# Optimization experiments

Hardware: AMD Instinct MI355X
Metric: run time of the kernel (lower is better)

The kernel has to match this reference:

```python
import jax, jax.numpy as jnp
import numpy as np

N_NODES = 50000
N_EDGES = 800000
N_ATOMS = 100
HID = 128
N_LAYERS = 3
OUT_LAYERS = 2
OUT_DIM = 1
N_GRAPHS = 1024
EPS = 1e-12  # F.normalize eps


def setup_inputs() -> dict:
    key = jax.random.key(0)
    ks = jax.random.split(key, 12)
    s = 0.05
    x_ori = jax.random.randint(ks[0], (N_NODES,), 0, N_ATOMS)
    edge_index = jax.random.randint(ks[1], (2, N_EDGES), 0, N_NODES)
    edge_attr = jax.random.normal(ks[2], (N_EDGES, 1), jnp.float32)
    batch_ids = jnp.sort(jax.random.randint(ks[3], (N_NODES,), 0, N_GRAPHS))
    embd_w = jax.random.normal(ks[4], (N_ATOMS, HID), jnp.float32) * s
    gamma_w = jnp.ones((N_LAYERS, N_ATOMS, 1), jnp.float32)  # reset_parameters sets ones
    w_atom_W = jax.random.normal(ks[5], (N_LAYERS, HID, HID), jnp.float32) * s
    w_atom_b = jax.random.normal(ks[6], (N_LAYERS, HID), jnp.float32) * s
    lin_W = jax.random.normal(ks[7], (OUT_LAYERS, HID, HID), jnp.float32) * s
    lin_b = jax.random.normal(ks[8], (OUT_LAYERS, HID), jnp.float32) * s
    wp_W = jax.random.normal(ks[9], (HID, OUT_DIM), jnp.float32) * s
    wp_b = jax.random.normal(ks[10], (OUT_DIM,), jnp.float32) * s
    return dict(x_ori=x_ori, edge_index=edge_index, edge_attr=edge_attr,
                batch_ids=batch_ids, embd_w=embd_w, gamma_w=gamma_w,
                w_atom_W=w_atom_W, w_atom_b=w_atom_b, lin_W=lin_W, lin_b=lin_b,
                wp_W=wp_W, wp_b=wp_b)


def reference(x_ori, edge_index, edge_attr, batch_ids, embd_w, gamma_w,
              w_atom_W, w_atom_b, lin_W, lin_b, wp_W, wp_b):
    src, dst = edge_index[0], edge_index[1]
    x = embd_w[x_ori]  # [N, H]
    for l in range(N_LAYERS):
        h = jax.nn.relu(x @ w_atom_W[l] + w_atom_b[l])            # [N, H]
        gam = jax.nn.sigmoid(gamma_w[l])[x_ori][dst]              # [E, 1]
        ew = jnp.exp(-gam * edge_attr ** 2)                       # [E, 1]
        msg = ew * h[src]                                         # [E, H] gather+weight
        agg = jax.ops.segment_sum(msg, dst, num_segments=N_NODES) # scatter-add
        y = agg + x
        nrm = jnp.maximum(jnp.linalg.norm(y, axis=1, keepdims=True), EPS)
        x = y / nrm                                               # F.normalize(., 2, 1)
    for i in range(OUT_LAYERS):
        x = jax.nn.relu(x @ lin_W[i] + lin_b[i])
    m_x = jax.ops.segment_sum(x, batch_ids, num_segments=N_GRAPHS)  # [G, H]
    props = m_x @ wp_W + wp_b                                      # [G, 1]
    return jnp.squeeze(props, axis=1)                              # [G]
```

## Files before the change

### kernel.cpp

```cpp
#include <hip/hip_runtime.h>
#include <hip/hip_bf16.h>
#include <math.h>

typedef __hip_bfloat16 bf16;
typedef unsigned int uint;
typedef unsigned short ushort;
typedef __attribute__((ext_vector_type(8))) short short8;
typedef __attribute__((ext_vector_type(4))) float f32x4;

#define HID 128
#define NN 50000
#define NE 800000
#define NG 1024
#define NA 100
#define CAP 64

__device__ __forceinline__ uint bf16_rne_hi(float f) {
    uint u = __float_as_uint(f);
    return (u + 0x7fffu + ((u >> 16) & 1u)) & 0xffff0000u;
}
__device__ __forceinline__ uint pack_bf16x2(float lo, float hi) {
    return (bf16_rne_hi(lo) >> 16) | bf16_rne_hi(hi);
}
__device__ __forceinline__ ushort bf16_rne(float f) {
    uint u = __float_as_uint(f);
    return (ushort)((u + 0x7fffu + ((u >> 16) & 1u)) >> 16);
}
__device__ __forceinline__ float load_f(const void* p, int i, int f32) {
    return f32 ? ((const float*)p)[i]
               : __uint_as_float((uint)((const ushort*)p)[i] << 16);
}
__device__ __forceinline__ int detect_f32(const void* emb) {
    const ushort* p = (const ushort*)emb;
    int lane = threadIdx.x & 63;
    int bad0, bad1;
    {
        float v = __uint_as_float((uint)p[lane * 4] << 16);
        bad0 = (!(v == v) || fabsf(v) > 1e4f || (v != 0.0f && fabsf(v) < 1e-10f));
        float w = __uint_as_float((uint)p[lane * 4 + 2] << 16);
        bad1 = (!(w == w) || fabsf(w) > 1e4f || (w != 0.0f && fabsf(w) < 1e-10f));
    }
    int cnt = __popcll(__ballot(bad0)) + __popcll(__ballot(bad1));
    return cnt > 16;
}

#define EMB_BLKS   ((NN * 64) / 256)
#define PACKW_BLKS (5 * 16384 / 256)
#define CVT_CNT    (300 + 384 + 256 + 128 + 1)
#define CVT_BLKS   5
#define INITC_BLKS ((NN + 255) / 256)
#define PREP_B1    EMB_BLKS
#define PREP_B2    (PREP_B1 + PACKW_BLKS)
#define PREP_B3    (PREP_B2 + CVT_BLKS)
#define PREP_B4    (PREP_B3 + INITC_BLKS)
#define PREP_GRID  (PREP_B4 + 1)

__global__ void prep_k(const int* __restrict__ xo, const void* __restrict__ emb,
                       const void* __restrict__ gamw, const void* __restrict__ wAW,
                       const void* __restrict__ wAb, const void* __restrict__ linW,
                       const void* __restrict__ linb, const void* __restrict__ wpW,
                       const void* __restrict__ wpb,
                       uint* __restrict__ xb, ushort* __restrict__ Wp,
                       float* __restrict__ f_sgam, float* __restrict__ f_wAb,
                       float* __restrict__ f_linb, float* __restrict__ f_wp,
                       float* __restrict__ f_wpb, int* __restrict__ cursor,
                       int* __restrict__ flag) {
    int f32 = detect_f32(emb);
    int b = blockIdx.x, t = threadIdx.x;
    if (b < PREP_B1) {
        int g = b * 256 + t;
        int node = g >> 6, c2 = g & 63;
        int base = xo[node] * HID + c2 * 2;
        xb[g] = pack_bf16x2(load_f(emb, base, f32), load_f(emb, base + 1, f32));
    } else if (b < PREP_B2) {
        int t2 = (b - PREP_B1) * 256 + t;
        int i   = t2 & 7;
        int n   = (t2 >> 3) & 15;
        int q   = (t2 >> 7) & 3;
        int j16 = (t2 >> 9) & 7;
        int ks  = (t2 >> 12) & 3;
        int mat = t2 >> 14;
        int k = ks * 32 + q * 8 + i;
        int j = j16 * 16 + n;
        const void* W = (mat < 3) ? wAW : linW;
        int off = ((mat < 3) ? mat : (mat - 3)) * 16384 + k * HID + j;
        Wp[t2] = bf16_rne(load_f(W, off, f32));
    } else if (b < PREP_B3) {
        int idx = (b - PREP_B2) * 256 + t;
        if (idx < 300) {
            float v = load_f(gamw, idx, f32);
            f_sgam[idx] = 1.0f / (1.0f + __expf(-v));
        } else if (idx < 684) {
            f_wAb[idx - 300] = load_f(wAb, idx - 300, f32);
        } else if (idx < 940) {
            f_linb[idx - 684] = load_f(linb, idx - 684, f32);
        } else if (idx < 1068) {
            f_wp[idx - 940] = load_f(wpW, idx - 940, f32);
        } else if (idx < CVT_CNT) {
            f_wpb[0] = load_f(wpb, 0, f32);
        }
    } else if (b < PREP_B4) {
        int n = (b - PREP_B3) * 256 + t;
        if (n < NN) cursor[n] = n * CAP;
    } else {
        if (t == 0) *flag = f32;
    }
}

__global__ void scatter_k(const int* __restrict__ src, const int* __restrict__ dst,
                          const void* __restrict__ ea, int* __restrict__ cursor,
                          uint* __restrict__ csr, const int* __restrict__ flag) {
    int e0 = (blockIdx.x * blockDim.x + threadIdx.x) * 4;
    if (e0 >= NE) return;
    int4 s4 = *(const int4*)(src + e0);
    int4 d4 = *(const int4*)(dst + e0);
    float a0, a1, a2, a3;
    if (*flag) {
        float4 f = *(const float4*)((const float*)ea + e0);
        a0 = f.x; a1 = f.y; a2 = f.z; a3 = f.w;
    } else {
        ushort4 u = *(const ushort4*)((const ushort*)ea + e0);
        a0 = __uint_as_float((uint)u.x << 16);
        a1 = __uint_as_float((uint)u.y << 16);
        a2 = __uint_as_float((uint)u.z << 16);
        a3 = __uint_as_float((uint)u.w << 16);
    }
    int p0 = atomicAdd(&cursor[d4.x], 1);
    int p1 = atomicAdd(&cursor[d4.y], 1);
    int p2 = atomicAdd(&cursor[d4.z], 1);
    int p3 = atomicAdd(&cursor[d4.w], 1);
    if (p0 < d4.x * CAP + CAP) csr[p0] = (uint)(s4.x & 0xffff) | bf16_rne_hi(a0 * a0);
    if (p1 < d4.y * CAP + CAP) csr[p1] = (uint)(s4.y & 0xffff) | bf16_rne_hi(a1 * a1);
    if (p2 < d4.z * CAP + CAP) csr[p2] = (uint)(s4.z & 0xffff) | bf16_rne_hi(a2 * a2);
    if (p3 < d4.w * CAP + CAP) csr[p3] = (uint)(s4.w & 0xffff) | bf16_rne_hi(a3 * a3);
}

__global__ __launch_bounds__(256) void gemm_mfma_k(const uint* __restrict__ xb,
                                                   const ushort* __restrict__ Wp,
                                                   const float* __restrict__ bias,
                                                   uint* __restrict__ outb) {
    int wave = threadIdx.x >> 6;
    int lane = threadIdx.x & 63;
    int ln15 = lane & 15;
    int q    = lane >> 4;
    int m0   = blockIdx.x * 128 + wave * 32;
    int mA = min(m0 + ln15, NN - 1);
    int mB = min(m0 + 16 + ln15, NN - 1);

    const short8* A8 = (const short8*)xb;
    const short8* B8 = (const short8*)Wp;

    f32x4 acc0[8], acc1[8];
#pragma unroll
    for (int j16 = 0; j16 < 8; ++j16) {
        float bv = bias[j16 * 16 + ln15];
        acc0[j16] = (f32x4){bv, bv, bv, bv};
        acc1[j16] = acc0[j16];
    }
#pragma unroll
    for (int ks = 0; ks < 4; ++ks) {
        short8 a0 = A8[mA * 16 + ks * 4 + q];
        short8 a1 = A8[mB * 16 + ks * 4 + q];
#pragma unroll
        for (int j16 = 0; j16 < 8; ++j16) {
            short8 b = B8[(ks * 8 + j16) * 64 + q * 16 + ln15];
            acc0[j16] = __builtin_amdgcn_mfma_f32_16x16x32_bf16(a0, b, acc0[j16], 0, 0, 0);
            acc1[j16] = __builtin_amdgcn_mfma_f32_16x16x32_bf16(a1, b, acc1[j16], 0, 0, 0);
        }
    }
    ushort* ob = (ushort*)outb;
#pragma unroll
    for (int reg = 0; reg < 4; ++reg) {
        int n0 = m0 + q * 4 + reg;
        int n1 = n0 + 16;
#pragma unroll
        for (int j16 = 0; j16 < 8; ++j16) {
            if (n0 < NN)
                ob[(size_t)n0 * HID + j16 * 16 + ln15] = bf16_rne(fmaxf(acc0[j16][reg], 0.0f));
            if (n1 < NN)
                ob[(size_t)n1 * HID + j16 * 16 + ln15] = bf16_rne(fmaxf(acc1[j16][reg], 0.0f));
        }
    }
}

__global__ void gather_norm_k(const int* __restrict__ cursor, const uint* __restrict__ csr,
                              const int* __restrict__ xo, const float* __restrict__ sgam,
                              const uint* __restrict__ hb, uint* __restrict__ xb) {
    int n = blockIdx.x * 4 + (threadIdx.x >> 6);
    int lane = threadIdx.x & 63;
    int base = n * CAP;
    int deg = min(cursor[n] - base, CAP);
    const uint* cp = csr + base;
    float g = sgam[xo[n]];
    float ax = 0.0f, ay = 0.0f;
    for (int e = 0; e < deg; e += 8) {
        uint4 c0 = *(const uint4*)(cp + e);
        uint4 c1 = *(const uint4*)(cp + e + 4);
        uint cc[8];
        cc[0] = c0.x; cc[1] = c0.y; cc[2] = c0.z; cc[3] = c0.w;
        cc[4] = c1.x; cc[5] = c1.y; cc[6] = c1.z; cc[7] = c1.w;
#pragma unroll
        for (int i = 1; i < 8; ++i) cc[i] = (e + i < deg) ? cc[i] : cc[0];
        uint v[8];
#pragma unroll
        for (int i = 0; i < 8; ++i) v[i] = hb[(cc[i] & 0xffffu) * 64 + lane];
        float w[8];
#pragma unroll
        for (int i = 0; i < 8; ++i) {
            float we = __expf(-g * __uint_as_float(cc[i] & 0xffff0000u));
            w[i] = (e + i < deg) ? we : 0.0f;
        }
#pragma unroll
        for (int i = 0; i < 8; ++i) {
            ax = fmaf(w[i], __uint_as_float(v[i] << 16), ax);
            ay = fmaf(w[i], __uint_as_float(v[i] & 0xffff0000u), ay);
        }
    }
    uint xv = xb[n * 64 + lane];
    float yx = ax + __uint_as_float(xv << 16);
    float yy = ay + __uint_as_float(xv & 0xffff0000u);
    float ss = yx * yx + yy * yy;
#pragma unroll
    for (int m = 32; m; m >>= 1) ss += __shfl_xor(ss, m);
    float inv = 1.0f / fmaxf(sqrtf(ss), 1e-12f);
    xb[n * 64 + lane] = pack_bf16x2(yx * inv, yy * inv);
}

__global__ void graph_k(const uint* __restrict__ xb, const int* __restrict__ batch,
                        const float* __restrict__ wp, const float* __restrict__ wpb,
                        void* __restrict__ out, const int* __restrict__ flag) {
    int g = blockIdx.x, tid = threadIdx.x;
    int lo = 0, hi = NN;
    while (lo < hi) { int mid = (lo + hi) >> 1; if (batch[mid] < g) lo = mid + 1; else hi = mid; }
    int start = lo;
    hi = NN;
    while (lo < hi) { int mid = (lo + hi) >> 1; if (batch[mid] < g + 1) lo = mid + 1; else hi = mid; }
    int end = lo;
    int c2 = tid & 63, half = tid >> 6;
    float wp0 = wp[c2 * 2], wp1 = wp[c2 * 2 + 1];
    float acc = 0.0f;
    for (int n = start + half; n < end; n += 2) {
        uint v = xb[(size_t)n * 64 + c2];
        acc = fmaf(__uint_as_float(v << 16), wp0, acc);
        acc = fmaf(__uint_as_float(v & 0xffff0000u), wp1, acc);
    }
    __shared__ float red[128];
    red[tid] = acc;
    __syncthreads();
#pragma unroll
    for (int s = 64; s; s >>= 1) {
        if (tid < s) red[tid] += red[tid + s];
        __syncthreads();
    }
    if (tid == 0) {
        float r = red[0] + wpb[0];
        if (*flag) ((float*)out)[g] = r;
        else       ((bf16*)out)[g] = __float2bfloat16(r);
    }
}

extern "C" void kernel_launch(void* const* d_in, const int* in_sizes, int n_in,
                              void* d_out, int out_size, void* d_ws, size_t ws_size,
                              hipStream_t stream) {
    const int*  xo    = (const int*)d_in[0];
    const int*  ei    = (const int*)d_in[1];
    const int*  src   = ei;
    const int*  dst   = ei + NE;
    const void* ea    = d_in[2];
    const int*  batch = (const int*)d_in[3];
    const void* emb   = d_in[4];
    const void* gamw  = d_in[5];
    const void* wAW   = d_in[6];
    const void* wAb   = d_in[7];
    const void* linW  = d_in[8];
    const void* linb  = d_in[9];
    const void* wpW   = d_in[10];
    const void* wpb   = d_in[11];

    float* F = (float*)d_ws;
    uint*  xb     = (uint*)F;
    uint*  hb     = xb + (size_t)NN * 64;
    uint*  csr    = hb + (size_t)NN * 64;
    int*   cursor = (int*)(csr + (size_t)NN * CAP);
    float* P      = (float*)(cursor + NN + 7);
    float* f_sgam = P;
    float* f_wAb  = f_sgam + 304;
    float* f_linb = f_wAb + 384;
    float* f_wp   = f_linb + 256;
    float* f_wpb  = f_wp + 128;
    int*   flag   = (int*)(f_wpb + 8);
    ushort* Wp    = (ushort*)(flag + 8);

    prep_k<<<PREP_GRID, 256, 0, stream>>>(xo, emb, gamw, wAW, wAb, linW, linb, wpW, wpb,
                                          xb, Wp, f_sgam, f_wAb, f_linb, f_wp, f_wpb,
                                          cursor, flag);

    scatter_k<<<(NE / 4 + 255) / 256, 256, 0, stream>>>(src, dst, ea, cursor, csr, flag);

    const int gemm_grid = (NN + 127) / 128;
    for (int l = 0; l < 3; ++l) {
        gemm_mfma_k<<<gemm_grid, 256, 0, stream>>>(xb, Wp + l * 16384, f_wAb + l * HID, hb);
        gather_norm_k<<<NN / 4, 256, 0, stream>>>(cursor, csr, xo, f_sgam + l * NA,
                                                  hb, xb);
    }

    gemm_mfma_k<<<gemm_grid, 256, 0, stream>>>(xb, Wp + 3 * 16384, f_linb,       hb);
    gemm_mfma_k<<<gemm_grid, 256, 0, stream>>>(hb, Wp + 4 * 16384, f_linb + HID, xb);

    graph_k<<<NG, 128, 0, stream>>>(xb, batch, f_wp, f_wpb, d_out, flag);
}
```

Measured before the change: 324.0 us.

## Build CSR via two-pass shared-memory binning instead of global atomics

Replaces the per-edge global atomic scatter into the fixed-capacity CSR with two passes. The first pass stages edges in shared memory, grouped into 98 coarse destination buckets, and flushes each bucket to global memory with one atomic per bucket. The second pass has each block own a 128-node quarter of a bucket, builds its CSR slice with shared-memory atomics, and writes it out with coalesced stores. This is meant to cut the contention and scattered writes of global atomics. In exchange it adds an intermediate bin buffer, an extra kernel launch, and a redundant scan in which each of four blocks reads the whole bucket.

```diff
diff --git a/kernel.cpp b/kernel.cpp
--- a/kernel.cpp
+++ b/kernel.cpp
@@ -14,6 +14,11 @@
 #define NG 1024
 #define NA 100
 #define CAP 64
+
+#define NB   98
+#define BCAP 16384
+#define SCAP 32
+#define NN_PAD (NB * 512)
 
 __device__ __forceinline__ uint bf16_rne_hi(float f) {
     uint u = __float_as_uint(f);
@@ -46,14 +51,12 @@
 
 #define EMB_BLKS   ((NN * 64) / 256)
 #define PACKW_BLKS (5 * 16384 / 256)
-#define CVT_CNT    (300 + 384 + 256 + 128 + 1)
+#define CVT_CNT    (300 + 384 + 256 + 128 + 1 + NB)
 #define CVT_BLKS   5
-#define INITC_BLKS ((NN + 255) / 256)
 #define PREP_B1    EMB_BLKS
 #define PREP_B2    (PREP_B1 + PACKW_BLKS)
 #define PREP_B3    (PREP_B2 + CVT_BLKS)
-#define PREP_B4    (PREP_B3 + INITC_BLKS)
-#define PREP_GRID  (PREP_B4 + 1)
+#define PREP_GRID  (PREP_B3 + 1)
 
 __global__ void prep_k(const int* __restrict__ xo, const void* __restrict__ emb,
                        const void* __restrict__ gamw, const void* __restrict__ wAW,
@@ -63,7 +66,7 @@
                        uint* __restrict__ xb, ushort* __restrict__ Wp,
                        float* __restrict__ f_sgam, float* __restrict__ f_wAb,
                        float* __restrict__ f_linb, float* __restrict__ f_wp,
-                       float* __restrict__ f_wpb, int* __restrict__ cursor,
+                       float* __restrict__ f_wpb, int* __restrict__ gcur,
                        int* __restrict__ flag) {
     int f32 = detect_f32(emb);
     int b = blockIdx.x, t = threadIdx.x;
@@ -96,43 +99,94 @@
             f_linb[idx - 684] = load_f(linb, idx - 684, f32);
         } else if (idx < 1068) {
             f_wp[idx - 940] = load_f(wpW, idx - 940, f32);
+        } else if (idx < 1069) {
+            f_wpb[0] = load_f(wpb, 0, f32);
         } else if (idx < CVT_CNT) {
-            f_wpb[0] = load_f(wpb, 0, f32);
-        }
-    } else if (b < PREP_B4) {
-        int n = (b - PREP_B3) * 256 + t;
-        if (n < NN) cursor[n] = n * CAP;
+            gcur[idx - 1069] = (idx - 1069) * BCAP;
+        }
     } else {
         if (t == 0) *flag = f32;
     }
 }
 
-__global__ void scatter_k(const int* __restrict__ src, const int* __restrict__ dst,
-                          const void* __restrict__ ea, int* __restrict__ cursor,
-                          uint* __restrict__ csr, const int* __restrict__ flag) {
-    int e0 = (blockIdx.x * blockDim.x + threadIdx.x) * 4;
-    if (e0 >= NE) return;
-    int4 s4 = *(const int4*)(src + e0);
-    int4 d4 = *(const int4*)(dst + e0);
-    float a0, a1, a2, a3;
-    if (*flag) {
-        float4 f = *(const float4*)((const float*)ea + e0);
-        a0 = f.x; a1 = f.y; a2 = f.z; a3 = f.w;
-    } else {
-        ushort4 u = *(const ushort4*)((const ushort*)ea + e0);
-        a0 = __uint_as_float((uint)u.x << 16);
-        a1 = __uint_as_float((uint)u.y << 16);
-        a2 = __uint_as_float((uint)u.z << 16);
-        a3 = __uint_as_float((uint)u.w << 16);
-    }
-    int p0 = atomicAdd(&cursor[d4.x], 1);
-    int p1 = atomicAdd(&cursor[d4.y], 1);
-    int p2 = atomicAdd(&cursor[d4.z], 1);
-    int p3 = atomicAdd(&cursor[d4.w], 1);
-    if (p0 < d4.x * CAP + CAP) csr[p0] = (uint)(s4.x & 0xffff) | bf16_rne_hi(a0 * a0);
-    if (p1 < d4.y * CAP + CAP) csr[p1] = (uint)(s4.y & 0xffff) | bf16_rne_hi(a1 * a1);
-    if (p2 < d4.z * CAP + CAP) csr[p2] = (uint)(s4.z & 0xffff) | bf16_rne_hi(a2 * a2);
-    if (p3 < d4.w * CAP + CAP) csr[p3] = (uint)(s4.w & 0xffff) | bf16_rne_hi(a3 * a3);
+__global__ __launch_bounds__(256) void binA_k(const int* __restrict__ src,
+                                              const int* __restrict__ dst,
+                                              const void* __restrict__ ea,
+                                              int* __restrict__ gcur,
+                                              uint2* __restrict__ bin,
+                                              const int* __restrict__ flag) {
+    __shared__ uint2 stage[NB][SCAP];
+    __shared__ int scnt[NB];
+    int t = threadIdx.x, wave = t >> 6, lane = t & 63;
+    int f32 = *flag;
+    for (int i = t; i < NB; i += 256) scnt[i] = 0;
+    __syncthreads();
+    for (int c = blockIdx.x; c * 1024 < NE; c += gridDim.x) {
+        int base = c * 1024;
+#pragma unroll
+        for (int i = 0; i < 4; ++i) {
+            int e = base + i * 256 + t;
+            if (e < NE) {
+                int d = dst[e];
+                int s = src[e];
+                float a = f32 ? ((const float*)ea)[e]
+                              : __uint_as_float((uint)((const ushort*)ea)[e] << 16);
+                uint2 en = make_uint2((uint)d, (uint)(s & 0xffff) | bf16_rne_hi(a * a));
+                int bk = d >> 9;
+                int pos = atomicAdd(&scnt[bk], 1);
+                if (pos < SCAP) {
+                    stage[bk][pos] = en;
+                } else {
+                    int g = atomicAdd(&gcur[bk], 1);
+                    if (g < (bk + 1) * BCAP) bin[g] = en;
+                }
+            }
+        }
+        __syncthreads();
+        for (int bk = wave; bk < NB; bk += 4) {
+            int cnt = min(scnt[bk], SCAP);
+            if (cnt > 0) {
+                int gpos = 0;
+                if (lane == 0) gpos = atomicAdd(&gcur[bk], cnt);
+                gpos = __shfl(gpos, 0);
+                if (lane < cnt && gpos + lane < (bk + 1) * BCAP)
+                    bin[gpos + lane] = stage[bk][lane];
+            }
+        }
+        __syncthreads();
+        for (int i = t; i < NB; i += 256) scnt[i] = 0;
+        __syncthreads();
+    }
+}
+
+__global__ __launch_bounds__(256) void binB_k(const int* __restrict__ gcur,
+                                              const uint2* __restrict__ bin,
+                                              uint* __restrict__ csr,
+                                              int* __restrict__ cursor) {
+    __shared__ uint lcsr[128 * CAP];
+    __shared__ int lcnt[128];
+    int t = threadIdx.x;
+    int b1 = blockIdx.x >> 2, qtr = blockIdx.x & 3;
+    int lo = b1 * 512 + qtr * 128;
+    if (t < 128) lcnt[t] = 0;
+    __syncthreads();
+    int cnt = min(gcur[b1] - b1 * BCAP, BCAP);
+    const uint2* bp = bin + (size_t)b1 * BCAP;
+    for (int i = t; i < cnt; i += 256) {
+        uint2 en = bp[i];
+        int loc = (int)en.x - lo;
+        if ((unsigned)loc < 128u) {
+            int p = atomicAdd(&lcnt[loc], 1);
+            if (p < CAP) lcsr[loc * CAP + p] = en.y;
+        }
+    }
+    __syncthreads();
+    uint* cbase = csr + (size_t)lo * CAP;
+    for (int i = t; i < 128 * CAP; i += 256) cbase[i] = lcsr[i];
+    if (t < 128) {
+        int n = lo + t;
+        if (n < NN) cursor[n] = n * CAP + min(lcnt[t], CAP);
+    }
 }
 
 __global__ __launch_bounds__(256) void gemm_mfma_k(const uint* __restrict__ xb,
@@ -277,11 +331,11 @@
     const void* wpW   = d_in[10];
     const void* wpb   = d_in[11];
 
-    float* F = (float*)d_ws;
-    uint*  xb     = (uint*)F;
+    uint*  xb     = (uint*)d_ws;
     uint*  hb     = xb + (size_t)NN * 64;
     uint*  csr    = hb + (size_t)NN * 64;
-    int*   cursor = (int*)(csr + (size_t)NN * CAP);
+    uint2* bin    = (uint2*)(csr + (size_t)NN_PAD * CAP);
+    int*   cursor = (int*)(bin + (size_t)NB * BCAP);
     float* P      = (float*)(cursor + NN + 7);
     float* f_sgam = P;
     float* f_wAb  = f_sgam + 304;
@@ -289,13 +343,15 @@
     float* f_wp   = f_linb + 256;
     float* f_wpb  = f_wp + 128;
     int*   flag   = (int*)(f_wpb + 8);
-    ushort* Wp    = (ushort*)(flag + 8);
+    int*   gcur   = flag + 8;
+    ushort* Wp    = (ushort*)(gcur + NB + 2);
 
     prep_k<<<PREP_GRID, 256, 0, stream>>>(xo, emb, gamw, wAW, wAb, linW, linb, wpW, wpb,
                                           xb, Wp, f_sgam, f_wAb, f_linb, f_wp, f_wpb,
-                                          cursor, flag);
-
-    scatter_k<<<(NE / 4 + 255) / 256, 256, 0, stream>>>(src, dst, ea, cursor, csr, flag);
+                                          gcur, flag);
+
+    binA_k<<<512, 256, 0, stream>>>(src, dst, ea, gcur, bin, flag);
+    binB_k<<<NB * 4, 256, 0, stream>>>(gcur, bin, csr, cursor);
 
     const int gemm_grid = (NN + 127) / 128;
     for (int l = 0; l < 3; ++l) {
```

Measured after the change: 770.6 us. 138% more time.

## Co-schedule edge scatter with first GEMM and fuse last GEMM with graph pooling

Applied to the files above, without the earlier changes.

The edge-to-CSR scatter now runs in the same launch as the layer-0 GEMM, with disjoint block ranges, so the two independent jobs overlap. The final output GEMM computes the dot product with the prediction weights in registers and atomically adds per-node results into per-graph accumulators. This replaces the separate graph reduction kernel, which did a binary search per graph and re-read the activations. The cost is float atomics, which make the summation order nondeterministic, plus an extra zeroing pass and a tiny output kernel.

```diff
diff --git a/kernel.cpp b/kernel.cpp
--- a/kernel.cpp
+++ b/kernel.cpp
@@ -33,13 +33,10 @@
 __device__ __forceinline__ int detect_f32(const void* emb) {
     const ushort* p = (const ushort*)emb;
     int lane = threadIdx.x & 63;
-    int bad0, bad1;
-    {
-        float v = __uint_as_float((uint)p[lane * 4] << 16);
-        bad0 = (!(v == v) || fabsf(v) > 1e4f || (v != 0.0f && fabsf(v) < 1e-10f));
-        float w = __uint_as_float((uint)p[lane * 4 + 2] << 16);
-        bad1 = (!(w == w) || fabsf(w) > 1e4f || (w != 0.0f && fabsf(w) < 1e-10f));
-    }
+    float v = __uint_as_float((uint)p[lane * 4] << 16);
+    int bad0 = (!(v == v) || fabsf(v) > 1e4f || (v != 0.0f && fabsf(v) < 1e-10f));
+    float w = __uint_as_float((uint)p[lane * 4 + 2] << 16);
+    int bad1 = (!(w == w) || fabsf(w) > 1e4f || (w != 0.0f && fabsf(w) < 1e-10f));
     int cnt = __popcll(__ballot(bad0)) + __popcll(__ballot(bad1));
     return cnt > 16;
 }
@@ -53,7 +50,8 @@
 #define PREP_B2    (PREP_B1 + PACKW_BLKS)
 #define PREP_B3    (PREP_B2 + CVT_BLKS)
 #define PREP_B4    (PREP_B3 + INITC_BLKS)
-#define PREP_GRID  (PREP_B4 + 1)
+#define PREP_B5    (PREP_B4 + 4)
+#define PREP_GRID  (PREP_B5 + 1)
 
 __global__ void prep_k(const int* __restrict__ xo, const void* __restrict__ emb,
                        const void* __restrict__ gamw, const void* __restrict__ wAW,
@@ -64,7 +62,7 @@
                        float* __restrict__ f_sgam, float* __restrict__ f_wAb,
                        float* __restrict__ f_linb, float* __restrict__ f_wp,
                        float* __restrict__ f_wpb, int* __restrict__ cursor,
-                       int* __restrict__ flag) {
+                       float* __restrict__ grf, int* __restrict__ flag) {
     int f32 = detect_f32(emb);
     int b = blockIdx.x, t = threadIdx.x;
     if (b < PREP_B1) {
@@ -102,55 +100,24 @@
     } else if (b < PREP_B4) {
         int n = (b - PREP_B3) * 256 + t;
         if (n < NN) cursor[n] = n * CAP;
+    } else if (b < PREP_B5) {
+        grf[(b - PREP_B4) * 256 + t] = 0.0f;
     } else {
         if (t == 0) *flag = f32;
     }
 }
 
-__global__ void scatter_k(const int* __restrict__ src, const int* __restrict__ dst,
-                          const void* __restrict__ ea, int* __restrict__ cursor,
-                          uint* __restrict__ csr, const int* __restrict__ flag) {
-    int e0 = (blockIdx.x * blockDim.x + threadIdx.x) * 4;
-    if (e0 >= NE) return;
-    int4 s4 = *(const int4*)(src + e0);
-    int4 d4 = *(const int4*)(dst + e0);
-    float a0, a1, a2, a3;
-    if (*flag) {
-        float4 f = *(const float4*)((const float*)ea + e0);
-        a0 = f.x; a1 = f.y; a2 = f.z; a3 = f.w;
-    } else {
-        ushort4 u = *(const ushort4*)((const ushort*)ea + e0);
-        a0 = __uint_as_float((uint)u.x << 16);
-        a1 = __uint_as_float((uint)u.y << 16);
-        a2 = __uint_as_float((uint)u.z << 16);
-        a3 = __uint_as_float((uint)u.w << 16);
-    }
-    int p0 = atomicAdd(&cursor[d4.x], 1);
-    int p1 = atomicAdd(&cursor[d4.y], 1);
-    int p2 = atomicAdd(&cursor[d4.z], 1);
-    int p3 = atomicAdd(&cursor[d4.w], 1);
-    if (p0 < d4.x * CAP + CAP) csr[p0] = (uint)(s4.x & 0xffff) | bf16_rne_hi(a0 * a0);
-    if (p1 < d4.y * CAP + CAP) csr[p1] = (uint)(s4.y & 0xffff) | bf16_rne_hi(a1 * a1);
-    if (p2 < d4.z * CAP + CAP) csr[p2] = (uint)(s4.z & 0xffff) | bf16_rne_hi(a2 * a2);
-    if (p3 < d4.w * CAP + CAP) csr[p3] = (uint)(s4.w & 0xffff) | bf16_rne_hi(a3 * a3);
-}
-
-__global__ __launch_bounds__(256) void gemm_mfma_k(const uint* __restrict__ xb,
-                                                   const ushort* __restrict__ Wp,
-                                                   const float* __restrict__ bias,
-                                                   uint* __restrict__ outb) {
-    int wave = threadIdx.x >> 6;
-    int lane = threadIdx.x & 63;
+__device__ __forceinline__ void gemm_core(const uint* __restrict__ xb,
+                                          const ushort* __restrict__ Wp,
+                                          const float* __restrict__ bias,
+                                          int m0, int lane,
+                                          f32x4 acc0[8], f32x4 acc1[8]) {
     int ln15 = lane & 15;
     int q    = lane >> 4;
-    int m0   = blockIdx.x * 128 + wave * 32;
     int mA = min(m0 + ln15, NN - 1);
     int mB = min(m0 + 16 + ln15, NN - 1);
-
     const short8* A8 = (const short8*)xb;
     const short8* B8 = (const short8*)Wp;
-
-    f32x4 acc0[8], acc1[8];
 #pragma unroll
     for (int j16 = 0; j16 < 8; ++j16) {
         float bv = bias[j16 * 16 + ln15];
@@ -168,6 +135,12 @@
             acc1[j16] = __builtin_amdgcn_mfma_f32_16x16x32_bf16(a1, b, acc1[j16], 0, 0, 0);
         }
     }
+}
+
+__device__ __forceinline__ void gemm_store(f32x4 acc0[8], f32x4 acc1[8],
+                                           int m0, int lane, uint* __restrict__ outb) {
+    int ln15 = lane & 15;
+    int q    = lane >> 4;
     ushort* ob = (ushort*)outb;
 #pragma unroll
     for (int reg = 0; reg < 4; ++reg) {
@@ -181,6 +154,103 @@
                 ob[(size_t)n1 * HID + j16 * 16 + ln15] = bf16_rne(fmaxf(acc1[j16][reg], 0.0f));
         }
     }
+}
+
+#define GEMM_BLKS ((NN + 127) / 128)
+__global__ __launch_bounds__(256) void gemm_mfma_k(const uint* __restrict__ xb,
+                                                   const ushort* __restrict__ Wp,
+                                                   const float* __restrict__ bias,
+                                                   uint* __restrict__ outb) {
+    f32x4 acc0[8], acc1[8];
+    int m0 = blockIdx.x * 128 + (threadIdx.x >> 6) * 32;
+    gemm_core(xb, Wp, bias, m0, threadIdx.x & 63, acc0, acc1);
+    gemm_store(acc0, acc1, m0, threadIdx.x & 63, outb);
+}
+
+#define SCAT_BLKS (NE / 4 / 256)
+__global__ __launch_bounds__(256) void work2_k(const uint* __restrict__ xb,
+                                               const ushort* __restrict__ Wp,
+                                               const float* __restrict__ bias,
+                                               uint* __restrict__ outb,
+                                               const int* __restrict__ esrc,
+                                               const int* __restrict__ edst,
+                                               const void* __restrict__ ea,
+                                               const void* __restrict__ emb,
+                                               int* __restrict__ cursor,
+                                               uint* __restrict__ csr) {
+    int b = blockIdx.x;
+    if (b < GEMM_BLKS) {
+        f32x4 acc0[8], acc1[8];
+        int m0 = b * 128 + (threadIdx.x >> 6) * 32;
+        gemm_core(xb, Wp, bias, m0, threadIdx.x & 63, acc0, acc1);
+        gemm_store(acc0, acc1, m0, threadIdx.x & 63, outb);
+    } else {
+        int f32 = detect_f32(emb);
+        int e0 = ((b - GEMM_BLKS) * 256 + threadIdx.x) * 4;
+        int4 s4 = *(const int4*)(esrc + e0);
+        int4 d4 = *(const int4*)(edst + e0);
+        float a0, a1, a2, a3;
+        if (f32) {
+            float4 f = *(const float4*)((const float*)ea + e0);
+            a0 = f.x; a1 = f.y; a2 = f.z; a3 = f.w;
+        } else {
+            ushort4 u = *(const ushort4*)((const ushort*)ea + e0);
+            a0 = __uint_as_float((uint)u.x << 16);
+            a1 = __uint_as_float((uint)u.y << 16);
+            a2 = __uint_as_float((uint)u.z << 16);
+            a3 = __uint_as_float((uint)u.w << 16);
+        }
+        int p0 = atomicAdd(&cursor[d4.x], 1);
+        int p1 = atomicAdd(&cursor[d4.y], 1);
+        int p2 = atomicAdd(&cursor[d4.z], 1);
+        int p3 = atomicAdd(&cursor[d4.w], 1);
+        if (p0 < d4.x * CAP + CAP) csr[p0] = (uint)(s4.x & 0xffff) | bf16_rne_hi(a0 * a0);
+        if (p1 < d4.y * CAP + CAP) csr[p1] = (uint)(s4.y & 0xffff) | bf16_rne_hi(a1 * a1);
+        if (p2 < d4.z * CAP + CAP) csr[p2] = (uint)(s4.z & 0xffff) | bf16_rne_hi(a2 * a2);
+        if (p3 < d4.w * CAP + CAP) csr[p3] = (uint)(s4.w & 0xffff) | bf16_rne_hi(a3 * a3);
+    }
+}
+
+__global__ __launch_bounds__(256) void gemm5_graph_k(const uint* __restrict__ xb,
+                                                     const ushort* __restrict__ Wp,
+                                                     const float* __restrict__ bias,
+                                                     const float* __restrict__ wp,
+                                                     const int* __restrict__ batch,
+                                                     float* __restrict__ grf) {
+    int lane = threadIdx.x & 63;
+    int ln15 = lane & 15;
+    int q    = lane >> 4;
+    int m0 = blockIdx.x * 128 + (threadIdx.x >> 6) * 32;
+    f32x4 acc0[8], acc1[8];
+    gemm_core(xb, Wp, bias, m0, lane, acc0, acc1);
+    float wpv[8];
+#pragma unroll
+    for (int j16 = 0; j16 < 8; ++j16) wpv[j16] = wp[j16 * 16 + ln15];
+#pragma unroll
+    for (int half = 0; half < 2; ++half) {
+#pragma unroll
+        for (int reg = 0; reg < 4; ++reg) {
+            float s = 0.0f;
+#pragma unroll
+            for (int j16 = 0; j16 < 8; ++j16) {
+                float v = half ? acc1[j16][reg] : acc0[j16][reg];
+                s = fmaf(fmaxf(v, 0.0f), wpv[j16], s);
+            }
+#pragma unroll
+            for (int m = 1; m < 16; m <<= 1) s += __shfl_xor(s, m);
+            int n = m0 + half * 16 + q * 4 + reg;
+            if (ln15 == 0 && n < NN) atomicAdd(&grf[batch[n]], s);
+        }
+    }
+}
+
+__global__ void out_k(const float* __restrict__ grf, const float* __restrict__ wpb,
+                      void* __restrict__ out, const int* __restrict__ flag) {
+    int g = blockIdx.x * 256 + threadIdx.x;
+    if (g >= NG) return;
+    float r = grf[g] + wpb[0];
+    if (*flag) ((float*)out)[g] = r;
+    else       ((bf16*)out)[g] = __float2bfloat16(r);
 }
 
 __global__ void gather_norm_k(const int* __restrict__ cursor, const uint* __restrict__ csr,
@@ -224,39 +294,6 @@
     for (int m = 32; m; m >>= 1) ss += __shfl_xor(ss, m);
     float inv = 1.0f / fmaxf(sqrtf(ss), 1e-12f);
     xb[n * 64 + lane] = pack_bf16x2(yx * inv, yy * inv);
-}
-
-__global__ void graph_k(const uint* __restrict__ xb, const int* __restrict__ batch,
-                        const float* __restrict__ wp, const float* __restrict__ wpb,
-                        void* __restrict__ out, const int* __restrict__ flag) {
-    int g = blockIdx.x, tid = threadIdx.x;
-    int lo = 0, hi = NN;
-    while (lo < hi) { int mid = (lo + hi) >> 1; if (batch[mid] < g) lo = mid + 1; else hi = mid; }
-    int start = lo;
-    hi = NN;
-    while (lo < hi) { int mid = (lo + hi) >> 1; if (batch[mid] < g + 1) lo = mid + 1; else hi = mid; }
-    int end = lo;
-    int c2 = tid & 63, half = tid >> 6;
-    float wp0 = wp[c2 * 2], wp1 = wp[c2 * 2 + 1];
-    float acc = 0.0f;
-    for (int n = start + half; n < end; n += 2) {
-        uint v = xb[(size_t)n * 64 + c2];
-        acc = fmaf(__uint_as_float(v << 16), wp0, acc);
-        acc = fmaf(__uint_as_float(v & 0xffff0000u), wp1, acc);
-    }
-    __shared__ float red[128];
-    red[tid] = acc;
-    __syncthreads();
-#pragma unroll
-    for (int s = 64; s; s >>= 1) {
-        if (tid < s) red[tid] += red[tid + s];
-        __syncthreads();
-    }
-    if (tid == 0) {
-        float r = red[0] + wpb[0];
-        if (*flag) ((float*)out)[g] = r;
-        else       ((bf16*)out)[g] = __float2bfloat16(r);
-    }
 }
 
 extern "C" void kernel_launch(void* const* d_in, const int* in_sizes, int n_in,
@@ -277,12 +314,12 @@
     const void* wpW   = d_in[10];
     const void* wpb   = d_in[11];
 
-    float* F = (float*)d_ws;
-    uint*  xb     = (uint*)F;
+    uint*  xb     = (uint*)d_ws;
     uint*  hb     = xb + (size_t)NN * 64;
     uint*  csr    = hb + (size_t)NN * 64;
     int*   cursor = (int*)(csr + (size_t)NN * CAP);
-    float* P      = (float*)(cursor + NN + 7);
+    float* grf    = (float*)(cursor + NN);
+    float* P      = grf + NG;
     float* f_sgam = P;
     float* f_wAb  = f_sgam + 304;
     float* f_linb = f_wAb + 384;
@@ -293,19 +330,20 @@
 
     prep_k<<<PREP_GRID, 256, 0, stream>>>(xo, emb, gamw, wAW, wAb, linW, linb, wpW, wpb,
                                           xb, Wp, f_sgam, f_wAb, f_linb, f_wp, f_wpb,
-                                          cursor, flag);
-
-    scatter_k<<<(NE / 4 + 255) / 256, 256, 0, stream>>>(src, dst, ea, cursor, csr, flag);
-
-    const int gemm_grid = (NN + 127) / 128;
-    for (int l = 0; l < 3; ++l) {
-        gemm_mfma_k<<<gemm_grid, 256, 0, stream>>>(xb, Wp + l * 16384, f_wAb + l * HID, hb);
+                                          cursor, grf, flag);
+
+    work2_k<<<GEMM_BLKS + SCAT_BLKS, 256, 0, stream>>>(xb, Wp, f_wAb, hb,
+                                                       src, dst, ea, emb, cursor, csr);
+    gather_norm_k<<<NN / 4, 256, 0, stream>>>(cursor, csr, xo, f_sgam, hb, xb);
+
+    for (int l = 1; l < 3; ++l) {
+        gemm_mfma_k<<<GEMM_BLKS, 256, 0, stream>>>(xb, Wp + l * 16384, f_wAb + l * HID, hb);
         gather_norm_k<<<NN / 4, 256, 0, stream>>>(cursor, csr, xo, f_sgam + l * NA,
                                                   hb, xb);
     }
 
-    gemm_mfma_k<<<gemm_grid, 256, 0, stream>>>(xb, Wp + 3 * 16384, f_linb,       hb);
-    gemm_mfma_k<<<gemm_grid, 256, 0, stream>>>(hb, Wp + 4 * 16384, f_linb + HID, xb);
-
-    graph_k<<<NG, 128, 0, stream>>>(xb, batch, f_wp, f_wpb, d_out, flag);
-}
+    gemm_mfma_k<<<GEMM_BLKS, 256, 0, stream>>>(xb, Wp + 3 * 16384, f_linb, hb);
+    gemm5_graph_k<<<GEMM_BLKS, 256, 0, stream>>>(hb, Wp + 4 * 16384, f_linb + HID,
+                                                 f_wp, batch, grf);
+    out_k<<<(NG + 255) / 256, 256, 0, stream>>>(grf, f_wpb, d_out, flag);
+}
```

After: 310.9 us. 1.04x faster.
